# Kernel tuning notes

Hardware: AMD Instinct MI355X
Metric: run time of the kernel (lower is better)

Reference implementation:

```python
import jax, jax.numpy as jnp
import numpy as np
from jax import lax

D = 512
K = 5
HID = 2 * D
EPS = 1e-5


def layernorm(x, g, b):
    mu = jnp.mean(x, axis=-1, keepdims=True)
    var = jnp.mean((x - mu) ** 2, axis=-1, keepdims=True)
    return (x - mu) * lax.rsqrt(var + EPS) * g + b


def setup_inputs() -> dict:
    key = jax.random.key(0)
    ks = jax.random.split(key, 16)
    B, T = 8, 4096
    sc = lambda fan: 1.0 / np.sqrt(fan)
    return {
        "x": jax.random.normal(ks[0], (B, T, D), jnp.float32),
        "decay_logit": jnp.zeros((D,), jnp.float32),
        "W_out": jax.random.uniform(ks[1], (D, D), jnp.float32, -sc(D), sc(D)),
        "b_out": jax.random.uniform(ks[2], (D,), jnp.float32, -sc(D), sc(D)),
        "conv_w": jax.random.uniform(ks[3], (D, 1, K), jnp.float32, -sc(K), sc(K)),
        "conv_b": jax.random.uniform(ks[4], (D,), jnp.float32, -sc(K), sc(K)),
        "ln1_g": jnp.ones((D,), jnp.float32),
        "ln1_b": jnp.zeros((D,), jnp.float32),
        "ln2_g": jnp.ones((D,), jnp.float32),
        "ln2_b": jnp.zeros((D,), jnp.float32),
        "W1": jax.random.uniform(ks[5], (HID, D), jnp.float32, -sc(D), sc(D)),
        "b1": jax.random.uniform(ks[6], (HID,), jnp.float32, -sc(D), sc(D)),
        "W2": jax.random.uniform(ks[7], (D, HID), jnp.float32, -sc(HID), sc(HID)),
        "b2": jax.random.uniform(ks[8], (D,), jnp.float32, -sc(HID), sc(HID)),
    }


def retention_core(xn, decay_logit, W_out, b_out, conv_w, conv_b):
    # xn: [B, T, D]
    B, T, _ = xn.shape
    a = jax.nn.sigmoid(decay_logit)  # [D]

    def step(s, xt):  # s, xt: [B, D]
        s = a * s + (1.0 - a) * xt
        return s, s

    s0 = jnp.zeros((B, D), xn.dtype)
    _, ss = lax.scan(step, s0, jnp.swapaxes(xn, 0, 1))  # [T, B, D]
    ss = jnp.swapaxes(ss, 0, 1)  # [B, T, D]
    y_ret = jnp.einsum("btd,ed->bte", ss, W_out) + b_out

    # depthwise conv1d, 'same' padding (K odd)
    xc = jnp.swapaxes(xn, 1, 2)  # [B, D, T]
    pad = (K - 1) // 2
    y_loc = lax.conv_general_dilated(
        xc, conv_w, window_strides=(1,), padding=[(pad, pad)],
        feature_group_count=D, dimension_numbers=("NCH", "OIH", "NCH"))
    y_loc = jnp.swapaxes(y_loc + conv_b[None, :, None], 1, 2)  # [B, T, D]
    return y_ret + y_loc


def reference(x, decay_logit, W_out, b_out, conv_w, conv_b,
              ln1_g, ln1_b, ln2_g, ln2_b, W1, b1, W2, b2):
    y = retention_core(layernorm(x, ln1_g, ln1_b),
                       decay_logit, W_out, b_out, conv_w, conv_b)
    x = x + y
    h = layernorm(x, ln2_g, ln2_b)
    h = jax.nn.gelu(jnp.einsum("btd,hd->bth", h, W1) + b1, approximate=False)
    y = jnp.einsum("bth,dh->btd", h, W2) + b2
    return x + y
```

## Files before the change

### kernel.cpp

```cpp
#include <hip/hip_runtime.h>
#include <stdint.h>

typedef unsigned short u16;

#define DIM 512
#define HIDN 1024
#define TT 4096
#define BB 8
#define MM 32768
#define CH 128
#define CL 32

__device__ __forceinline__ u16 f2bf(float f) {
  union { float f; uint32_t u; } v; v.f = f;
  uint32_t u = v.u;
  uint32_t r = u + 0x7fffu + ((u >> 16) & 1u);
  return (u16)(r >> 16);
}
__device__ __forceinline__ float bf2f(u16 h) {
  union { uint32_t u; float f; } v; v.u = ((uint32_t)h) << 16; return v.f;
}

typedef __bf16 bf16x8 __attribute__((ext_vector_type(8)));
typedef float f32x4 __attribute__((ext_vector_type(4)));

__global__ __launch_bounds__(256) void prep_kernel(
    const float* __restrict__ wout, const float* __restrict__ w1,
    const float* __restrict__ w2, const float* __restrict__ dl,
    const float* __restrict__ convw,
    u16* __restrict__ wout_h, u16* __restrict__ w1_h, u16* __restrict__ w2_h,
    float* __restrict__ a, float* __restrict__ oma, float* __restrict__ aL,
    float* __restrict__ convwT) {
  int i = blockIdx.x * 256 + threadIdx.x;
  if (i < DIM * DIM) wout_h[i] = f2bf(wout[i]);
  if (i < HIDN * DIM) { w1_h[i] = f2bf(w1[i]); w2_h[i] = f2bf(w2[i]); }
  if (i < 5 * DIM) {
    int kk = i / DIM, n = i - kk * DIM;
    convwT[i] = convw[n * 5 + kk];
  }
  if (i < DIM) {
    float av = 1.0f / (1.0f + expf(-dl[i]));
    a[i] = av; oma[i] = 1.0f - av; aL[i] = powf(av, (float)CL);
  }
}

__global__ __launch_bounds__(256) void ln_rows(
    const float* __restrict__ xin, const float* __restrict__ g,
    const float* __restrict__ bvec, u16* __restrict__ out) {
  int lane = threadIdx.x & 63, wave = threadIdx.x >> 6;
  size_t row = (size_t)blockIdx.x * 4 + wave;
  const float4* xr = (const float4*)(xin + row * DIM);
  float4 v0 = xr[lane * 2 + 0];
  float4 v1 = xr[lane * 2 + 1];
  float s1 = v0.x + v0.y + v0.z + v0.w + v1.x + v1.y + v1.z + v1.w;
  float s2 = v0.x * v0.x + v0.y * v0.y + v0.z * v0.z + v0.w * v0.w
           + v1.x * v1.x + v1.y * v1.y + v1.z * v1.z + v1.w * v1.w;
#pragma unroll
  for (int o = 1; o < 64; o <<= 1) { s1 += __shfl_xor(s1, o); s2 += __shfl_xor(s2, o); }
  float mu = s1 * (1.0f / DIM);
  float var = s2 * (1.0f / DIM) - mu * mu;
  float rs = rsqrtf(var + 1e-5f);
  const float4* gr = (const float4*)g;
  const float4* br = (const float4*)bvec;
  float4 g0 = gr[lane * 2], g1 = gr[lane * 2 + 1];
  float4 b0 = br[lane * 2], b1 = br[lane * 2 + 1];
  uint32_t p0 = (uint32_t)f2bf((v0.x - mu) * rs * g0.x + b0.x) | ((uint32_t)f2bf((v0.y - mu) * rs * g0.y + b0.y) << 16);
  uint32_t p1 = (uint32_t)f2bf((v0.z - mu) * rs * g0.z + b0.z) | ((uint32_t)f2bf((v0.w - mu) * rs * g0.w + b0.w) << 16);
  uint32_t p2 = (uint32_t)f2bf((v1.x - mu) * rs * g1.x + b1.x) | ((uint32_t)f2bf((v1.y - mu) * rs * g1.y + b1.y) << 16);
  uint32_t p3 = (uint32_t)f2bf((v1.z - mu) * rs * g1.z + b1.z) | ((uint32_t)f2bf((v1.w - mu) * rs * g1.w + b1.w) << 16);
  uint4 pk; pk.x = p0; pk.y = p1; pk.z = p2; pk.w = p3;
  ((uint4*)(out + row * DIM))[lane] = pk;
}

__global__ __launch_bounds__(256) void scan_local(
    const u16* __restrict__ xn, const float* __restrict__ a,
    const float* __restrict__ oma, float* __restrict__ carry) {
  int idx = blockIdx.x * 256 + threadIdx.x;
  int dp = (idx & 255) * 2;
  int c = (idx >> 8) & (CH - 1);
  int b = idx >> 15;
  float a0 = a[dp], a1 = a[dp + 1], o0 = oma[dp], o1 = oma[dp + 1];
  const uint32_t* xp = (const uint32_t*)(xn + ((size_t)(b * TT + c * CL)) * DIM + dp);
  float s0 = 0.f, s1 = 0.f;
#pragma unroll
  for (int i = 0; i < CL; ++i) {
    uint32_t u = xp[(size_t)i * (DIM / 2)];
    s0 = fmaf(a0, s0, o0 * bf2f((u16)(u & 0xffffu)));
    s1 = fmaf(a1, s1, o1 * bf2f((u16)(u >> 16)));
  }
  float2 cv; cv.x = s0; cv.y = s1;
  *(float2*)&carry[((size_t)(b * CH + c)) * DIM + dp] = cv;
}

__global__ __launch_bounds__(256) void scan_carry(
    const float* __restrict__ carry, const float* __restrict__ aL,
    float* __restrict__ start) {
  int idx = blockIdx.x * 256 + threadIdx.x;
  int d = idx & (DIM - 1);
  int b = idx >> 9;
  float al = aL[d];
  float s = 0.f;
#pragma unroll 8
  for (int c = 0; c < CH; ++c) {
    size_t o = ((size_t)(b * CH + c)) * DIM + d;
    start[o] = s;
    s = fmaf(al, s, carry[o]);
  }
}

__global__ __launch_bounds__(256) void scan_emit(
    const u16* __restrict__ xn, const float* __restrict__ a,
    const float* __restrict__ oma, const float* __restrict__ start,
    u16* __restrict__ ss) {
  int idx = blockIdx.x * 256 + threadIdx.x;
  int dp = (idx & 255) * 2;
  int c = (idx >> 8) & (CH - 1);
  int b = idx >> 15;
  float a0 = a[dp], a1 = a[dp + 1], o0 = oma[dp], o1 = oma[dp + 1];
  const uint32_t* xp = (const uint32_t*)(xn + ((size_t)(b * TT + c * CL)) * DIM + dp);
  uint32_t* sp = (uint32_t*)(ss + ((size_t)(b * TT + c * CL)) * DIM + dp);
  float2 st = *(const float2*)&start[((size_t)(b * CH + c)) * DIM + dp];
  float s0 = st.x, s1 = st.y;
#pragma unroll
  for (int i = 0; i < CL; ++i) {
    uint32_t u = xp[(size_t)i * (DIM / 2)];
    s0 = fmaf(a0, s0, o0 * bf2f((u16)(u & 0xffffu)));
    s1 = fmaf(a1, s1, o1 * bf2f((u16)(u >> 16)));
    sp[(size_t)i * (DIM / 2)] = (uint32_t)f2bf(s0) | ((uint32_t)f2bf(s1) << 16);
  }
}

template <int Kd, int NCOL, int EPI>
__global__ __launch_bounds__(512, 2) void gemm_bt(
    const u16* __restrict__ A, const u16* __restrict__ Bmat,
    const float* __restrict__ bias, const float* __restrict__ resid,
    const u16* __restrict__ xn, const float* __restrict__ convwT,
    const float* __restrict__ convb, float* __restrict__ outf,
    u16* __restrict__ outh) {
  extern __shared__ __align__(16) u16 lds[];
  u16* sAb = lds;
  u16* sBb = lds + 32768;
  const int tid = threadIdx.x;
  const int lane = tid & 63, wave = tid >> 6;
  const int wm = wave >> 2;
  const int wn = wave & 3;
  const int rA = lane & 15, q = lane >> 4;
  const int lrow = lane >> 3;
  const int lslot = lane & 7;
  const int gk = ((lslot ^ lrow) & 7) * 8;

  const int lin = blockIdx.x;
  const int tile_col = (lin >> 3) & (NCOL - 1);
  const int tile_row = (lin & 7) + 8 * ((lin >> 3) / NCOL);
  const size_t rowTile = (size_t)tile_row * 256;
  const size_t colTile = (size_t)tile_col * 256;

  const u16* Abase = A + rowTile * Kd;
  const u16* Bbase = Bmat + colTile * Kd;

  f32x4 acc[8][4];
#pragma unroll
  for (int i = 0; i < 8; i++)
#pragma unroll
    for (int j = 0; j < 4; j++) acc[i][j] = (f32x4){0.f, 0.f, 0.f, 0.f};

  auto stage = [&](int kt, int buf) {
#pragma unroll
    for (int j = 0; j < 4; ++j) {
      const int g = j * 8 + wave;
      const u16* ga = Abase + (size_t)(g * 8 + lrow) * Kd + kt + gk;
      const u16* gb = Bbase + (size_t)(g * 8 + lrow) * Kd + kt + gk;
      __builtin_amdgcn_global_load_lds(
          (const __attribute__((address_space(1))) void*)ga,
          (__attribute__((address_space(3))) void*)(sAb + buf * 16384 + g * 512), 16, 0, 0);
      __builtin_amdgcn_global_load_lds(
          (const __attribute__((address_space(1))) void*)gb,
          (__attribute__((address_space(3))) void*)(sBb + buf * 16384 + g * 512), 16, 0, 0);
    }
  };

  constexpr int NT = Kd / 64;
  stage(0, 0);
  __asm__ __volatile__("s_waitcnt vmcnt(0)" ::: "memory");
  __asm__ __volatile__("s_barrier" ::: "memory");

  const int sw = rA & 7;
#pragma unroll 1
  for (int t = 0; t < NT; ++t) {
    const int p = t & 1;
    const u16* bufA = sAb + p * 16384 + (wm * 128 + rA) * 64;
    const u16* bufB = sBb + p * 16384 + (wn * 64 + rA) * 64;

    if (t + 1 < NT) stage((t + 1) * 64, p ^ 1);

    bf16x8 bfr[4][2], afr[8][2];
#pragma unroll
    for (int ni = 0; ni < 4; ++ni)
#pragma unroll
      for (int ks = 0; ks < 2; ++ks)
        bfr[ni][ks] = *(const bf16x8*)&bufB[ni * 1024 + (((ks * 4 + q) ^ sw) * 8)];
#pragma unroll
    for (int mi = 0; mi < 2; ++mi)
#pragma unroll
      for (int ks = 0; ks < 2; ++ks)
        afr[mi][ks] = *(const bf16x8*)&bufA[mi * 1024 + (((ks * 4 + q) ^ sw) * 8)];

#pragma unroll
    for (int qd = 0; qd < 4; ++qd) {
      if (qd < 3) {
#pragma unroll
        for (int mi = 2 * qd + 2; mi < 2 * qd + 4; ++mi)
#pragma unroll
          for (int ks = 0; ks < 2; ++ks)
            afr[mi][ks] = *(const bf16x8*)&bufA[mi * 1024 + (((ks * 4 + q) ^ sw) * 8)];
      }
      __builtin_amdgcn_s_setprio(1);
#pragma unroll
      for (int mi = 2 * qd; mi < 2 * qd + 2; ++mi)
#pragma unroll
        for (int ni = 0; ni < 4; ++ni)
#pragma unroll
          for (int ks = 0; ks < 2; ++ks)
            acc[mi][ni] = __builtin_amdgcn_mfma_f32_16x16x32_bf16(bfr[ni][ks], afr[mi][ks], acc[mi][ni], 0, 0, 0);
      __builtin_amdgcn_s_setprio(0);
    }

    __asm__ __volatile__("s_waitcnt lgkmcnt(0) vmcnt(0)" ::: "memory");
    __asm__ __volatile__("s_barrier" ::: "memory");
  }

#pragma unroll
  for (int mi = 0; mi < 8; ++mi) {
    size_t m = rowTile + wm * 128 + mi * 16 + rA;
#pragma unroll
    for (int ni = 0; ni < 4; ++ni) {
      int n0 = (int)colTile + wn * 64 + ni * 16 + q * 4;
      f32x4 v = acc[mi][ni];
      float4 bv = *(const float4*)&bias[n0];
      float val0 = v[0] + bv.x, val1 = v[1] + bv.y, val2 = v[2] + bv.z, val3 = v[3] + bv.w;
      if constexpr (EPI == 0) {
        int tt = (int)(m & (TT - 1));
        float4 cb = *(const float4*)&convb[n0];
        float4 rv = *(const float4*)&resid[m * DIM + n0];
        val0 += cb.x + rv.x; val1 += cb.y + rv.y; val2 += cb.z + rv.z; val3 += cb.w + rv.w;
#pragma unroll
        for (int kk = 0; kk < 5; ++kk) {
          int ttc = tt + kk - 2;
          if (ttc >= 0 && ttc < TT) {
            uint2 xv = *(const uint2*)&xn[(m + (size_t)kk - 2) * DIM + n0];
            float4 wv = *(const float4*)&convwT[kk * DIM + n0];
            val0 = fmaf(wv.x, bf2f((u16)(xv.x & 0xffffu)), val0);
            val1 = fmaf(wv.y, bf2f((u16)(xv.x >> 16)), val1);
            val2 = fmaf(wv.z, bf2f((u16)(xv.y & 0xffffu)), val2);
            val3 = fmaf(wv.w, bf2f((u16)(xv.y >> 16)), val3);
          }
        }
        float4 ov; ov.x = val0; ov.y = val1; ov.z = val2; ov.w = val3;
        *(float4*)&outf[m * DIM + n0] = ov;
      } else if constexpr (EPI == 1) {
        const float isq2 = 0.70710678118654752f;
        float g0 = 0.5f * val0 * (1.0f + erff(val0 * isq2));
        float g1 = 0.5f * val1 * (1.0f + erff(val1 * isq2));
        float g2 = 0.5f * val2 * (1.0f + erff(val2 * isq2));
        float g3 = 0.5f * val3 * (1.0f + erff(val3 * isq2));
        uint2 pk;
        pk.x = (uint32_t)f2bf(g0) | ((uint32_t)f2bf(g1) << 16);
        pk.y = (uint32_t)f2bf(g2) | ((uint32_t)f2bf(g3) << 16);
        *(uint2*)&outh[m * HIDN + n0] = pk;
      } else {
        float4 rv = *(const float4*)&resid[m * DIM + n0];
        float4 ov;
        ov.x = val0 + rv.x; ov.y = val1 + rv.y; ov.z = val2 + rv.z; ov.w = val3 + rv.w;
        *(float4*)&outf[m * DIM + n0] = ov;
      }
    }
  }
}

extern "C" void kernel_launch(void* const* d_in, const int* in_sizes, int n_in,
                              void* d_out, int out_size, void* d_ws, size_t ws_size,
                              hipStream_t stream) {
  const float* x      = (const float*)d_in[0];
  const float* dl     = (const float*)d_in[1];
  const float* W_out  = (const float*)d_in[2];
  const float* b_out  = (const float*)d_in[3];
  const float* conv_w = (const float*)d_in[4];
  const float* conv_b = (const float*)d_in[5];
  const float* ln1_g  = (const float*)d_in[6];
  const float* ln1_b  = (const float*)d_in[7];
  const float* ln2_g  = (const float*)d_in[8];
  const float* ln2_b  = (const float*)d_in[9];
  const float* W1     = (const float*)d_in[10];
  const float* b1     = (const float*)d_in[11];
  const float* W2     = (const float*)d_in[12];
  const float* b2     = (const float*)d_in[13];

  char* ws = (char*)d_ws;
  u16*   wout_h = (u16*)(ws + 0);
  u16*   w1_h   = (u16*)(ws + 524288);
  u16*   w2_h   = (u16*)(ws + 1572864);
  float* a_buf  = (float*)(ws + 2621440);
  float* oma    = (float*)(ws + 2623488);
  float* aL     = (float*)(ws + 2625536);
  float* convwT = (float*)(ws + 2627584);
  float* carry  = (float*)(ws + (4u << 20));
  float* start  = (float*)(ws + 6291456);
  u16*   xn  = (u16*)(ws + (8u << 20));
  u16*   ssb = (u16*)(ws + (40u << 20));
  float* x1  = (float*)(ws + (72u << 20));
  u16*   h   = (u16*)(ws + (136u << 20));
  u16*   hg  = (u16*)(ws + (168u << 20));

  float* out = (float*)d_out;

  hipFuncSetAttribute(reinterpret_cast<const void*>(&gemm_bt<512, 2, 0>),
                      hipFuncAttributeMaxDynamicSharedMemorySize, 131072);
  hipFuncSetAttribute(reinterpret_cast<const void*>(&gemm_bt<512, 4, 1>),
                      hipFuncAttributeMaxDynamicSharedMemorySize, 131072);
  hipFuncSetAttribute(reinterpret_cast<const void*>(&gemm_bt<1024, 2, 2>),
                      hipFuncAttributeMaxDynamicSharedMemorySize, 131072);

  prep_kernel<<<2048, 256, 0, stream>>>(W_out, W1, W2, dl, conv_w, wout_h, w1_h, w2_h, a_buf, oma, aL, convwT);
  ln_rows<<<MM / 4, 256, 0, stream>>>(x, ln1_g, ln1_b, xn);
  scan_local<<<(BB * CH * DIM / 2) / 256, 256, 0, stream>>>(xn, a_buf, oma, carry);
  scan_carry<<<(BB * DIM) / 256, 256, 0, stream>>>(carry, aL, start);
  scan_emit<<<(BB * CH * DIM / 2) / 256, 256, 0, stream>>>(xn, a_buf, oma, start, ssb);
  gemm_bt<512, 2, 0><<<256, 512, 131072, stream>>>(ssb, wout_h, b_out, x, xn, convwT, conv_b, x1, nullptr);
  ln_rows<<<MM / 4, 256, 0, stream>>>(x1, ln2_g, ln2_b, h);
  gemm_bt<512, 4, 1><<<512, 512, 131072, stream>>>(h, w1_h, b1, nullptr, nullptr, nullptr, nullptr, nullptr, hg);
  gemm_bt<1024, 2, 2><<<256, 512, 131072, stream>>>(hg, w2_h, b2, x1, nullptr, nullptr, nullptr, out, nullptr);
}
```

Baseline: 466.4 us.

## Use four-stage LDS ring with 32-wide K slices in GEMM mainloop

Replaces the double-buffered 64-wide K staging with a four-slot ring of 32-wide K slices, prefetching three steps ahead. Waits become partial vmcnt counts, so earlier loads can still be in flight while the MFMAs run. The LDS swizzle changes to a 4-slot XOR pattern to fit the narrower rows. In exchange there are twice as many iterations and barriers, and the hand-coded vmcnt bookkeeping is fragile.

```diff
diff --git a/kernel.cpp b/kernel.cpp
--- a/kernel.cpp
+++ b/kernel.cpp
@@ -138,16 +138,16 @@
     const float* __restrict__ convb, float* __restrict__ outf,
     u16* __restrict__ outh) {
   extern __shared__ __align__(16) u16 lds[];
-  u16* sAb = lds;
-  u16* sBb = lds + 32768;
+  u16* sA = lds;
+  u16* sB = lds + 32768;
   const int tid = threadIdx.x;
   const int lane = tid & 63, wave = tid >> 6;
   const int wm = wave >> 2;
   const int wn = wave & 3;
   const int rA = lane & 15, q = lane >> 4;
-  const int lrow = lane >> 3;
-  const int lslot = lane & 7;
-  const int gk = ((lslot ^ lrow) & 7) * 8;
+
+  const int lrow4 = lane >> 2;
+  const int sg = (lane & 3) ^ ((lane >> 2) & 3) ^ ((lane >> 4) & 3);
 
   const int lin = blockIdx.x;
   const int tile_col = (lin >> 3) & (NCOL - 1);
@@ -164,68 +164,67 @@
 #pragma unroll
     for (int j = 0; j < 4; j++) acc[i][j] = (f32x4){0.f, 0.f, 0.f, 0.f};
 
-  auto stage = [&](int kt, int buf) {
-#pragma unroll
-    for (int j = 0; j < 4; ++j) {
-      const int g = j * 8 + wave;
-      const u16* ga = Abase + (size_t)(g * 8 + lrow) * Kd + kt + gk;
-      const u16* gb = Bbase + (size_t)(g * 8 + lrow) * Kd + kt + gk;
+  auto stageA = [&](int t) {
+    const int b = t & 3;
+#pragma unroll
+    for (int r = 0; r < 2; ++r) {
+      const int rb = r * 128 + wave * 16;
+      const u16* ga = Abase + (size_t)(rb + lrow4) * Kd + t * 32 + sg * 8;
       __builtin_amdgcn_global_load_lds(
           (const __attribute__((address_space(1))) void*)ga,
-          (__attribute__((address_space(3))) void*)(sAb + buf * 16384 + g * 512), 16, 0, 0);
+          (__attribute__((address_space(3))) void*)(sA + b * 8192 + rb * 32 + lane * 8), 16, 0, 0);
+    }
+  };
+  auto stageB = [&](int t) {
+    const int b = t & 3;
+#pragma unroll
+    for (int r = 0; r < 2; ++r) {
+      const int rb = r * 128 + wave * 16;
+      const u16* gb = Bbase + (size_t)(rb + lrow4) * Kd + t * 32 + sg * 8;
       __builtin_amdgcn_global_load_lds(
           (const __attribute__((address_space(1))) void*)gb,
-          (__attribute__((address_space(3))) void*)(sBb + buf * 16384 + g * 512), 16, 0, 0);
+          (__attribute__((address_space(3))) void*)(sB + b * 8192 + rb * 32 + lane * 8), 16, 0, 0);
     }
   };
 
-  constexpr int NT = Kd / 64;
-  stage(0, 0);
-  __asm__ __volatile__("s_waitcnt vmcnt(0)" ::: "memory");
+  constexpr int NT = Kd / 32;
+  stageA(0); stageB(0);
+  stageA(1); stageB(1);
+  stageA(2); stageB(2);
+  __asm__ __volatile__("s_waitcnt vmcnt(8)" ::: "memory");
   __asm__ __volatile__("s_barrier" ::: "memory");
 
-  const int sw = rA & 7;
+  const int ps = (q ^ (rA & 3) ^ ((rA >> 2) & 3)) * 8;
+
 #pragma unroll 1
   for (int t = 0; t < NT; ++t) {
-    const int p = t & 1;
-    const u16* bufA = sAb + p * 16384 + (wm * 128 + rA) * 64;
-    const u16* bufB = sBb + p * 16384 + (wn * 64 + rA) * 64;
-
-    if (t + 1 < NT) stage((t + 1) * 64, p ^ 1);
-
-    bf16x8 bfr[4][2], afr[8][2];
-#pragma unroll
-    for (int ni = 0; ni < 4; ++ni)
-#pragma unroll
-      for (int ks = 0; ks < 2; ++ks)
-        bfr[ni][ks] = *(const bf16x8*)&bufB[ni * 1024 + (((ks * 4 + q) ^ sw) * 8)];
-#pragma unroll
-    for (int mi = 0; mi < 2; ++mi)
-#pragma unroll
-      for (int ks = 0; ks < 2; ++ks)
-        afr[mi][ks] = *(const bf16x8*)&bufA[mi * 1024 + (((ks * 4 + q) ^ sw) * 8)];
-
-#pragma unroll
-    for (int qd = 0; qd < 4; ++qd) {
-      if (qd < 3) {
-#pragma unroll
-        for (int mi = 2 * qd + 2; mi < 2 * qd + 4; ++mi)
-#pragma unroll
-          for (int ks = 0; ks < 2; ++ks)
-            afr[mi][ks] = *(const bf16x8*)&bufA[mi * 1024 + (((ks * 4 + q) ^ sw) * 8)];
-      }
-      __builtin_amdgcn_s_setprio(1);
-#pragma unroll
-      for (int mi = 2 * qd; mi < 2 * qd + 2; ++mi)
-#pragma unroll
-        for (int ni = 0; ni < 4; ++ni)
-#pragma unroll
-          for (int ks = 0; ks < 2; ++ks)
-            acc[mi][ni] = __builtin_amdgcn_mfma_f32_16x16x32_bf16(bfr[ni][ks], afr[mi][ks], acc[mi][ni], 0, 0, 0);
-      __builtin_amdgcn_s_setprio(0);
+    const int slot = t & 3;
+    const u16* bA = sA + slot * 8192 + (wm * 128 + rA) * 32 + ps;
+    const u16* bB = sB + slot * 8192 + (wn * 64 + rA) * 32 + ps;
+    bf16x8 bfr[4], afr[8];
+#pragma unroll
+    for (int ni = 0; ni < 4; ++ni) bfr[ni] = *(const bf16x8*)&bB[ni * 512];
+#pragma unroll
+    for (int mi = 0; mi < 8; ++mi) afr[mi] = *(const bf16x8*)&bA[mi * 512];
+
+    if (t + 3 < NT) { stageA(t + 3); stageB(t + 3); }
+
+    __builtin_amdgcn_s_setprio(1);
+#pragma unroll
+    for (int mi = 0; mi < 8; ++mi)
+#pragma unroll
+      for (int ni = 0; ni < 4; ++ni)
+        acc[mi][ni] = __builtin_amdgcn_mfma_f32_16x16x32_bf16(bfr[ni], afr[mi], acc[mi][ni], 0, 0, 0);
+    __builtin_amdgcn_s_setprio(0);
+
+    if (t < NT - 3) {
+      __asm__ __volatile__("s_waitcnt vmcnt(8)" ::: "memory");
+    } else if (t == NT - 3) {
+      __asm__ __volatile__("s_waitcnt vmcnt(4)" ::: "memory");
+    } else if (t == NT - 2) {
+      __asm__ __volatile__("s_waitcnt vmcnt(0)" ::: "memory");
     }
-
-    __asm__ __volatile__("s_waitcnt lgkmcnt(0) vmcnt(0)" ::: "memory");
+    __asm__ __volatile__("s_waitcnt lgkmcnt(0)" ::: "memory");
     __asm__ __volatile__("s_barrier" ::: "memory");
   }
 
```

Measured after the change: 393.6 us. 1.19x faster.
